# Optimization experiments

Measured on AMD Instinct MI355X. Metric: run time of the kernel, lower is better.

Reference implementation:

```python
import jax, jax.numpy as jnp
import numpy as np

B, S, HID = 2, 2048, 2048
NH, NKV, HD = 16, 4, 128  # num_heads, num_kv_heads, head_dim; kqv_size = NH*HD = 2048
KV_DIM = NKV * HD  # 512


def setup_inputs() -> dict:
    key = jax.random.key(0)
    ks = jax.random.split(key, 7)
    sc = 0.02
    return {
        "hidden_states": jax.random.normal(ks[0], (B, S, HID), dtype=jnp.float32),
        "Wq": jax.random.normal(ks[1], (NH * HD, HID), dtype=jnp.float32) * sc,
        "Wk": jax.random.normal(ks[2], (KV_DIM, HID), dtype=jnp.float32) * sc,
        "Wv": jax.random.normal(ks[3], (KV_DIM, HID), dtype=jnp.float32) * sc,
        "Wo": jax.random.normal(ks[4], (HID, NH * HD), dtype=jnp.float32) * sc,
        "bo": jnp.zeros((HID,), dtype=jnp.float32),
    }


def reference(hidden_states, Wq, Wk, Wv, Wo, bo):
    b, s, _ = hidden_states.shape
    # projections (nn.Linear: x @ W.T), no bias on q/k/v
    q = (hidden_states @ Wq.T).reshape(b, s, NH, HD).transpose(0, 2, 1, 3)   # [B,NH,S,HD]
    k = (hidden_states @ Wk.T).reshape(b, s, NKV, HD).transpose(0, 2, 1, 3)  # [B,NKV,S,HD]
    v = (hidden_states @ Wv.T).reshape(b, s, NKV, HD).transpose(0, 2, 1, 3)
    # GQA: query head h uses kv head h // (NH // NKV)
    g = NH // NKV
    k_rep = jnp.repeat(k, g, axis=1)  # [B,NH,S,HD]
    v_rep = jnp.repeat(v, g, axis=1)
    # float32 upcast, NO 1/sqrt(d) scaling (GPT-Neo style)
    qf = q.astype(jnp.float32)
    kf = k_rep.astype(jnp.float32)
    scores = jnp.einsum("bhqd,bhkd->bhqk", qf, kf)  # [B,NH,S,S]
    causal = jnp.tril(jnp.ones((s, s), dtype=bool))[None, None]
    neg = jnp.finfo(scores.dtype).min
    scores = jnp.where(causal, scores, neg)
    attn = jax.nn.softmax(scores, axis=-1).astype(v.dtype)  # dropout p=0 (eval)
    out = jnp.einsum("bhqk,bhkd->bhqd", attn, v_rep)         # [B,NH,S,HD]
    out = out.transpose(0, 2, 1, 3).reshape(b, s, NH * HD)
    return out @ Wo.T + bo
```

## Files before the change

### kernel.cpp

```cpp
#include <hip/hip_runtime.h>

typedef _Float16 f16;
typedef __attribute__((ext_vector_type(4))) _Float16 f16x4;
typedef __attribute__((ext_vector_type(8))) _Float16 f16x8;
typedef __attribute__((ext_vector_type(4))) float f32x4;

#define NB 2
#define NS 2048
#define NHID 2048
#define N_H 16
#define N_KV 4
#define N_HD 128

__device__ __forceinline__ void gload16(void* lds, const void* g) {
  __builtin_amdgcn_global_load_lds(
      (const __attribute__((address_space(1))) unsigned int*)g,
      (__attribute__((address_space(3))) unsigned int*)lds, 16, 0, 0);
}

__global__ __launch_bounds__(256) void cvt_kernel(const float* __restrict__ in,
                                                  f16* __restrict__ out, int n4) {
  int i = blockIdx.x * 256 + threadIdx.x;
  if (i >= n4) return;
  const float4 v = reinterpret_cast<const float4*>(in)[i];
  f16x4 o = {(f16)v.x, (f16)v.y, (f16)v.z, (f16)v.w};
  reinterpret_cast<f16x4*>(out)[i] = o;
}

__global__ __launch_bounds__(256) void cvt3_kernel(const float* __restrict__ a, int na4,
                                                   const float* __restrict__ b, int nb4,
                                                   const float* __restrict__ c, int nc4,
                                                   f16* __restrict__ out) {
  int i = blockIdx.x * 256 + threadIdx.x;
  if (i >= na4 + nb4 + nc4) return;
  const float* src;
  int j;
  if (i < na4) { src = a; j = i; }
  else if (i < na4 + nb4) { src = b; j = i - na4; }
  else { src = c; j = i - na4 - nb4; }
  const float4 v = reinterpret_cast<const float4*>(src)[j];
  f16x4 o = {(f16)v.x, (f16)v.y, (f16)v.z, (f16)v.w};
  reinterpret_cast<f16x4*>(out)[i] = o;
}

template <int MREP, int MODE>
__global__ __launch_bounds__(512, 2) void gemm8(
    const f16* __restrict__ A, const f16* __restrict__ Bm, const int K,
    f16* __restrict__ q_out, f16* __restrict__ k_out, f16* __restrict__ v_out,
    float* __restrict__ f_out, const float* __restrict__ bias) {
  constexpr int BM = MREP * 32;
  constexpr int GA = BM / 128;
  constexpr int G = GA + 2;
  constexpr int NPH = (MREP == 8) ? 2 : 1;
  constexpr int ATILE = BM * 32;
  constexpr int BTILE = 256 * 32;
  constexpr int BUF = ATILE + BTILE;
  __shared__ f16 lds[4 * BUF];

  const int t = threadIdx.x;
  const int l = t & 63, w = t >> 6;
  const int g = l >> 4, l15 = l & 15;
  const int wr = w >> 2, wc = w & 3;
  const int nb = blockIdx.x, mb = blockIdx.y;
  const int NT = K >> 5;

  const f16* Aorig = A + (size_t)(mb * BM) * K;
  const f16* Borig = Bm + (size_t)(nb * 256) * K;

  size_t offA[GA], offB[2];
#pragma unroll
  for (int gi = 0; gi < GA; ++gi) {
    int beta = gi * 8192 + t * 16;
    int r = ((beta >> 9) << 3) | ((beta >> 4) & 7);
    int c = (beta >> 7) & 3;
    offA[gi] = (size_t)r * K + c * 8;
  }
#pragma unroll
  for (int gj = 0; gj < 2; ++gj) {
    int beta = gj * 8192 + t * 16;
    int r = ((beta >> 9) << 3) | ((beta >> 4) & 7);
    int c = (beta >> 7) & 3;
    offB[gj] = (size_t)r * K + c * 8;
  }

  auto stage = [&](int kt, int gi) {
    f16* bufbase = lds + (kt & 3) * BUF;
    if (gi < GA) {
      gload16(bufbase + gi * 4096 + w * 512, Aorig + offA[gi] + kt * 32);
    } else {
      int gj = gi - GA;
      gload16(bufbase + ATILE + gj * 4096 + w * 512, Borig + offB[gj] + kt * 32);
    }
  };
  const int fragoff = ((l15 >> 3) << 8) + (g << 6) + ((l15 & 7) << 3);
  auto readA = [&](int kt, int mi) -> f16x8 {
    int R0 = wr * (MREP * 16) + mi * 16;
    return *reinterpret_cast<const f16x8*>(lds + (kt & 3) * BUF + R0 * 32 + fragoff);
  };
  auto readB = [&](int kt, int ni) -> f16x8 {
    int R0 = wc * 64 + ni * 16;
    return *reinterpret_cast<const f16x8*>(lds + (kt & 3) * BUF + ATILE + R0 * 32 + fragoff);
  };

  f32x4 acc[MREP][4] = {};

#pragma unroll
  for (int pt = 0; pt < 3; ++pt)
#pragma unroll
    for (int gi = 0; gi < G; ++gi) stage(pt, gi);
  if constexpr (MREP == 8) asm volatile("s_waitcnt vmcnt(8)" ::: "memory");
  else                     asm volatile("s_waitcnt vmcnt(6)" ::: "memory");
  __builtin_amdgcn_s_barrier();

  f16x8 bf[4];
  for (int kt = 0; kt < NT; ++kt) {
    const bool dostage = (kt + 3 < NT);
#pragma unroll
    for (int ph = 0; ph < NPH; ++ph) {
      f16x8 af[4];
#pragma unroll
      for (int mi = 0; mi < 4; ++mi) af[mi] = readA(kt, ph * 4 + mi);
      if (ph == 0) {
#pragma unroll
        for (int ni = 0; ni < 4; ++ni) bf[ni] = readB(kt, ni);
      }
      if (dostage) {
        if constexpr (NPH == 2) {
          stage(kt + 3, ph * 2);
          stage(kt + 3, ph * 2 + 1);
        } else {
          stage(kt + 3, 0);
          stage(kt + 3, 1);
          stage(kt + 3, 2);
        }
      }
      if (ph == NPH - 1) {
        if (kt + 3 < NT) {
          if constexpr (MREP == 8) asm volatile("s_waitcnt vmcnt(8)" ::: "memory");
          else                     asm volatile("s_waitcnt vmcnt(6)" ::: "memory");
        } else if (kt + 2 < NT) {
          if constexpr (MREP == 8) asm volatile("s_waitcnt vmcnt(4)" ::: "memory");
          else                     asm volatile("s_waitcnt vmcnt(3)" ::: "memory");
        } else if (kt + 1 < NT) {
          asm volatile("s_waitcnt vmcnt(0)" ::: "memory");
        }
      }
      __builtin_amdgcn_s_barrier();
      asm volatile("s_waitcnt lgkmcnt(0)" ::: "memory");
      __builtin_amdgcn_s_setprio(1);
#pragma unroll
      for (int mi = 0; mi < 4; ++mi)
#pragma unroll
        for (int ni = 0; ni < 4; ++ni)
          acc[ph * 4 + mi][ni] =
              __builtin_amdgcn_mfma_f32_16x16x32_f16(af[mi], bf[ni], acc[ph * 4 + mi][ni], 0, 0, 0);
      __builtin_amdgcn_s_setprio(0);
      __builtin_amdgcn_s_barrier();
    }
  }

#pragma unroll
  for (int mi = 0; mi < MREP; ++mi) {
    int m0 = mb * BM + wr * (MREP * 16) + mi * 16 + 4 * g;
#pragma unroll
    for (int ni = 0; ni < 4; ++ni) {
      int n = nb * 256 + wc * 64 + ni * 16 + l15;
#pragma unroll
      for (int r = 0; r < 4; ++r) {
        int mm = m0 + r;
        float val = acc[mi][ni][r];
        if (MODE == 0) {
          int b = mm >> 11, s = mm & (NS - 1);
          if (n < 2048) {
            int h = n >> 7, d = n & 127;
            q_out[(((size_t)(b * N_H + h)) * NS + s) * N_HD + d] = (f16)val;
          } else if (n < 2560) {
            int n2 = n - 2048, kvh = n2 >> 7, d = n2 & 127;
            k_out[(((size_t)(b * N_KV + kvh)) * NS + s) * N_HD + d] = (f16)val;
          } else {
            int n3 = n - 2560, kvh = n3 >> 7, d = n3 & 127;
            v_out[(((size_t)(b * N_KV + kvh)) * NS + s) * N_HD + d] = (f16)val;
          }
        } else {
          f_out[(size_t)mm * NHID + n] = val + bias[n];
        }
      }
    }
  }
}

__global__ __launch_bounds__(256) void transpose_v(const f16* __restrict__ V,
                                                   f16* __restrict__ Vt) {
  __shared__ f16 tt[64][72];
  int s0 = blockIdx.x * 64, d0 = blockIdx.y * 64, bk = blockIdx.z;
  const f16* Vp = V + (size_t)bk * NS * N_HD;
  f16* Vtp = Vt + (size_t)bk * N_HD * NS;
  int tid = threadIdx.x;
#pragma unroll
  for (int it = 0; it < 2; ++it) {
    int c = it * 256 + tid;
    int sr = c >> 3, dc = (c & 7) * 8;
    f16x8 v = *reinterpret_cast<const f16x8*>(Vp + (size_t)(s0 + sr) * N_HD + d0 + dc);
#pragma unroll
    for (int j = 0; j < 8; ++j) tt[dc + j][sr] = v[j];
  }
  __syncthreads();
#pragma unroll
  for (int it = 0; it < 2; ++it) {
    int c = it * 256 + tid;
    int dr = c >> 3, sc = (c & 7) * 8;
    f16x8 o;
#pragma unroll
    for (int j = 0; j < 8; ++j) o[j] = tt[dr][sc + j];
    *reinterpret_cast<f16x8*>(Vtp + (size_t)(d0 + dr) * NS + s0 + sc) = o;
  }
}

__device__ __forceinline__ void stage_kv(const f16* __restrict__ Kp,
                                         const f16* __restrict__ Vp,
                                         f16* Kl, f16* Vl, int kt, int w, int l) {
#pragma unroll
  for (int it = 0; it < 4; ++it) {
    int cb = (it * 4 + w) * 64;
    int c = cb + l;
    int krow = c >> 4, pch = c & 15;
    int sch = (pch & 8) | ((pch ^ krow) & 7);
    gload16(Kl + cb * 8, Kp + (size_t)(kt * 64 + krow) * N_HD + sch * 8);
  }
#pragma unroll
  for (int it = 0; it < 4; ++it) {
    int cb = (it * 4 + w) * 64;
    int c = cb + l;
    int drow = c >> 3, pch = c & 7;
    int sch = (pch ^ drow) & 7;
    gload16(Vl + cb * 8, Vp + (size_t)drow * NS + kt * 64 + sch * 8);
  }
}

__device__ __forceinline__ void attn_step(
    const f16x8* qf, f32x4* oacc, float* mrow, float* lrow, int q0, int kt,
    const f16* Kl, const f16* Vl, f16* Pw, int g, int l15, bool diag) {
  f32x4 sacc[4];
  __builtin_amdgcn_s_setprio(1);
#pragma unroll
  for (int nt = 0; nt < 4; ++nt) {
    f32x4 z = {0.f, 0.f, 0.f, 0.f};
#pragma unroll
    for (int ks = 0; ks < 4; ++ks) {
      int kr = nt * 16 + l15;
      int ch = ks * 4 + g;
      int sw = (ch & 8) | ((ch ^ kr) & 7);
      f16x8 kf = *reinterpret_cast<const f16x8*>(Kl + kr * 128 + sw * 8);
      z = __builtin_amdgcn_mfma_f32_16x16x32_f16(qf[ks], kf, z, 0, 0, 0);
    }
    sacc[nt] = z;
  }
  __builtin_amdgcn_s_setprio(0);

  float p[4][4], mx[4];
  bool need = false;
#pragma unroll
  for (int r = 0; r < 4; ++r) {
    int qg = q0 + r;
    float m = -3.0e38f;
#pragma unroll
    for (int nt = 0; nt < 4; ++nt) {
      float sv = sacc[nt][r];
      if (diag) {
        int kg = kt * 64 + nt * 16 + l15;
        if (kg > qg) sv = -3.0e38f;
      }
      p[nt][r] = sv;
      m = fmaxf(m, sv);
    }
#pragma unroll
    for (int off = 8; off >= 1; off >>= 1) m = fmaxf(m, __shfl_xor(m, off));
    mx[r] = m;
    need = need || (m > mrow[r] + 11.5f);
  }
  if (__any(need)) {
#pragma unroll
    for (int r = 0; r < 4; ++r) {
      float m2 = fmaxf(mrow[r], mx[r]);
      float alpha = __builtin_amdgcn_exp2f(mrow[r] - m2);
      mrow[r] = m2;
      lrow[r] *= alpha;
#pragma unroll
      for (int dt = 0; dt < 8; ++dt) oacc[dt][r] *= alpha;
    }
  }
#pragma unroll
  for (int r = 0; r < 4; ++r) {
    float rs = 0.f;
#pragma unroll
    for (int nt = 0; nt < 4; ++nt) {
      float pv = __builtin_amdgcn_exp2f(p[nt][r] - mrow[r]);
      p[nt][r] = pv;
      rs += pv;
    }
#pragma unroll
    for (int off = 8; off >= 1; off >>= 1) rs += __shfl_xor(rs, off);
    lrow[r] += rs;
  }

#pragma unroll
  for (int nt = 0; nt < 4; ++nt)
#pragma unroll
    for (int r = 0; r < 4; ++r) {
      int ql = 4 * g + r;
      int kp = nt * 16 + l15;
      int ch = kp >> 3;
      int idx = ql * 64 + (ch ^ (ql & 7)) * 8 + (kp & 7);
      Pw[idx] = (f16)p[nt][r];
    }
  asm volatile("s_waitcnt lgkmcnt(0)" ::: "memory");
  __builtin_amdgcn_sched_barrier(0);

  f16x8 pa[2];
#pragma unroll
  for (int ks2 = 0; ks2 < 2; ++ks2) {
    int ch = ks2 * 4 + g;
    pa[ks2] = *reinterpret_cast<const f16x8*>(&Pw[l15 * 64 + (ch ^ (l15 & 7)) * 8]);
  }
  __builtin_amdgcn_s_setprio(1);
#pragma unroll
  for (int dt = 0; dt < 8; ++dt)
#pragma unroll
    for (int ks2 = 0; ks2 < 2; ++ks2) {
      int d = dt * 16 + l15;
      int ch = ks2 * 4 + g;
      f16x8 vf = *reinterpret_cast<const f16x8*>(Vl + d * 64 + (ch ^ (d & 7)) * 8);
      oacc[dt] = __builtin_amdgcn_mfma_f32_16x16x32_f16(pa[ks2], vf, oacc[dt], 0, 0, 0);
    }
  __builtin_amdgcn_s_setprio(0);
}

__global__ __launch_bounds__(256, 2) void attn_kernel(
    const f16* __restrict__ Q, const f16* __restrict__ K,
    const f16* __restrict__ Vt, f16* __restrict__ O) {
  __shared__ f16 Klds[2][64 * 128];
  __shared__ f16 Vlds[2][128 * 64];
  __shared__ f16 Plds[4][16 * 64];
  const int t = threadIdx.x, l = t & 63, w = t >> 6;
  const int g = l >> 4, l15 = l & 15;
  const int pi = blockIdx.x;
  const int qtA = pi, qtB = 31 - pi;
  const int bh = blockIdx.y;
  const int b = bh >> 4, h = bh & 15;
  const int kvh = h >> 2;
  const f16* Qp = Q + ((size_t)(b * N_H + h)) * NS * N_HD;
  const f16* Kp = K + ((size_t)(b * N_KV + kvh)) * NS * N_HD;
  const f16* Vp = Vt + ((size_t)(b * N_KV + kvh)) * N_HD * NS;

  const f16 l2e = (f16)1.44269504f;
  f16x8 qfA[4], qfB[4];
  const int qrA = qtA * 64 + w * 16 + l15;
  const int qrB = qtB * 64 + w * 16 + l15;
#pragma unroll
  for (int ks = 0; ks < 4; ++ks) {
    qfA[ks] = *reinterpret_cast<const f16x8*>(Qp + (size_t)qrA * N_HD + ks * 32 + g * 8);
    qfB[ks] = *reinterpret_cast<const f16x8*>(Qp + (size_t)qrB * N_HD + ks * 32 + g * 8);
#pragma unroll
    for (int j = 0; j < 8; ++j) { qfA[ks][j] *= l2e; qfB[ks][j] *= l2e; }
  }

  f32x4 oA[8] = {}, oB[8] = {};
  float mA[4], lAr[4], mB[4], lBr[4];
#pragma unroll
  for (int r = 0; r < 4; ++r) {
    mA[r] = -3.0e38f; lAr[r] = 0.f;
    mB[r] = -3.0e38f; lBr[r] = 0.f;
  }
  const int q0A = qtA * 64 + w * 16 + 4 * g;
  const int q0B = qtB * 64 + w * 16 + 4 * g;

  const int nkt = qtB + 1;
  stage_kv(Kp, Vp, Klds[0], Vlds[0], 0, w, l);
  asm volatile("s_waitcnt vmcnt(0)" ::: "memory");
  __syncthreads();
  int cur = 0;
  for (int kt = 0; kt < nkt; ++kt) {
    if (kt + 1 < nkt)
      stage_kv(Kp, Vp, Klds[cur ^ 1], Vlds[cur ^ 1], kt + 1, w, l);
    attn_step(qfB, oB, mB, lBr, q0B, kt, Klds[cur], Vlds[cur], Plds[w], g, l15, kt == qtB);
    if (kt <= qtA)
      attn_step(qfA, oA, mA, lAr, q0A, kt, Klds[cur], Vlds[cur], Plds[w], g, l15, kt == qtA);
    asm volatile("s_waitcnt vmcnt(0)" ::: "memory");
    __syncthreads();
    cur ^= 1;
  }

#pragma unroll
  for (int r = 0; r < 4; ++r) {
    float invB = 1.0f / lBr[r];
    f16* orowB = O + (size_t)(b * NS + q0B + r) * NHID + h * N_HD;
#pragma unroll
    for (int dt = 0; dt < 8; ++dt) orowB[dt * 16 + l15] = (f16)(oB[dt][r] * invB);
    float invA = 1.0f / lAr[r];
    f16* orowA = O + (size_t)(b * NS + q0A + r) * NHID + h * N_HD;
#pragma unroll
    for (int dt = 0; dt < 8; ++dt) orowA[dt * 16 + l15] = (f16)(oA[dt][r] * invA);
  }
}

extern "C" void kernel_launch(void* const* d_in, const int* in_sizes, int n_in,
                              void* d_out, int out_size, void* d_ws, size_t ws_size,
                              hipStream_t stream) {
  const float* hs = (const float*)d_in[0];
  const float* Wq = (const float*)d_in[1];
  const float* Wk = (const float*)d_in[2];
  const float* Wv = (const float*)d_in[3];
  const float* Wo = (const float*)d_in[4];
  const float* bo = (const float*)d_in[5];
  float* out = (float*)d_out;

  char* ws = (char*)d_ws;
  f16* Xh   = (f16*)(ws);
  f16* Wqkv = (f16*)(ws + 16777216);
  f16* Woh  = (f16*)(ws + 29360128);
  f16* Qb   = (f16*)(ws + 37748736);
  f16* Kb   = (f16*)(ws + 54525952);
  f16* Vb   = (f16*)(ws + 58720256);
  f16* Vtb  = (f16*)(ws + 62914560);
  f16* Ob   = Xh;

  cvt_kernel<<<8192, 256, 0, stream>>>(hs, Xh, 2097152);
  cvt3_kernel<<<6144, 256, 0, stream>>>(Wq, 1048576, Wk, 262144, Wv, 262144, Wqkv);
  cvt_kernel<<<4096, 256, 0, stream>>>(Wo, Woh, 1048576);

  gemm8<8, 0><<<dim3(12, 16), 512, 0, stream>>>(Xh, Wqkv, 2048, Qb, Kb, Vb, nullptr, nullptr);
  transpose_v<<<dim3(32, 2, 8), 256, 0, stream>>>(Vb, Vtb);
  attn_kernel<<<dim3(16, 32), 256, 0, stream>>>(Qb, Kb, Vtb, Ob);
  gemm8<4, 1><<<dim3(8, 32), 512, 0, stream>>>(Ob, Woh, 2048, nullptr, nullptr, nullptr, out, bo);
}
```

Measured before the change: 239.8 us.

## Fuse conversions, add 256-block QKV GEMM, swizzle grids, simplify attention softmax

Merges the three fp32-to-fp16 conversion launches into one kernel. Replaces the QKV projection with a dedicated GEMM using 256x192 tiles and double-buffered 64-wide K steps, so the launch is 256 blocks. Remaps block indices in the QKV GEMM, output GEMM and attention kernel so that blocks sharing operand tiles or a KV head are launched together, aiming for better L2 reuse. In attention, the lazy-rescale branch is dropped in favour of always rescaling, row sums are computed with an MFMA against a ones vector instead of shuffles, and the setprio hints are removed. The trade-off is extra rescale work on every tile and a shallower load pipeline in the new GEMM.

```diff
diff --git a/kernel.cpp b/kernel.cpp
--- a/kernel.cpp
+++ b/kernel.cpp
@@ -18,35 +18,123 @@
       (__attribute__((address_space(3))) unsigned int*)lds, 16, 0, 0);
 }
 
-__global__ __launch_bounds__(256) void cvt_kernel(const float* __restrict__ in,
-                                                  f16* __restrict__ out, int n4) {
+__global__ __launch_bounds__(256) void cvt_all(
+    const float* __restrict__ hs, const float* __restrict__ Wq,
+    const float* __restrict__ Wk, const float* __restrict__ Wv,
+    const float* __restrict__ Wo, f16* __restrict__ Xh,
+    f16* __restrict__ Wqkv, f16* __restrict__ Woh) {
   int i = blockIdx.x * 256 + threadIdx.x;
-  if (i >= n4) return;
-  const float4 v = reinterpret_cast<const float4*>(in)[i];
-  f16x4 o = {(f16)v.x, (f16)v.y, (f16)v.z, (f16)v.w};
-  reinterpret_cast<f16x4*>(out)[i] = o;
-}
-
-__global__ __launch_bounds__(256) void cvt3_kernel(const float* __restrict__ a, int na4,
-                                                   const float* __restrict__ b, int nb4,
-                                                   const float* __restrict__ c, int nc4,
-                                                   f16* __restrict__ out) {
-  int i = blockIdx.x * 256 + threadIdx.x;
-  if (i >= na4 + nb4 + nc4) return;
   const float* src;
+  f16* dst;
   int j;
-  if (i < na4) { src = a; j = i; }
-  else if (i < na4 + nb4) { src = b; j = i - na4; }
-  else { src = c; j = i - na4 - nb4; }
+  if (i < 2097152)      { src = hs; dst = Xh;             j = i; }
+  else if (i < 3145728) { src = Wq; dst = Wqkv;           j = i - 2097152; }
+  else if (i < 3407872) { src = Wk; dst = Wqkv + 4194304; j = i - 3145728; }
+  else if (i < 3670016) { src = Wv; dst = Wqkv + 5242880; j = i - 3407872; }
+  else                  { src = Wo; dst = Woh;            j = i - 3670016; }
   const float4 v = reinterpret_cast<const float4*>(src)[j];
   f16x4 o = {(f16)v.x, (f16)v.y, (f16)v.z, (f16)v.w};
-  reinterpret_cast<f16x4*>(out)[i] = o;
+  reinterpret_cast<f16x4*>(dst)[j] = o;
+}
+
+__global__ __launch_bounds__(512, 2) void gemm_qkv(
+    const f16* __restrict__ A, const f16* __restrict__ Bm,
+    f16* __restrict__ q_out, f16* __restrict__ k_out, f16* __restrict__ v_out) {
+  constexpr int K = 2048;
+  __shared__ f16 lds[2][28672];
+  const int t = threadIdx.x;
+  const int l = t & 63, w = t >> 6;
+  const int g = l >> 4, l15 = l & 15;
+  const int wr = w >> 2, wc = w & 3;
+  const int orig = blockIdx.x;
+  const int x = orig & 7, loc = orig >> 3;
+  const int mb = (x & 3) * 4 + (loc & 3);
+  const int nb = (x >> 2) * 8 + (loc >> 2);
+  const f16* Ab = A + (size_t)(mb * 256) * K;
+  const f16* Bb = Bm + (size_t)(nb * 192) * K;
+
+  const int rA = ((t >> 5) << 3) | (t & 7);
+  const int cA = (t >> 3) & 3;
+  const int t2 = t & 255;
+  const int rB2 = ((t2 >> 5) << 3) | (t2 & 7);
+  const int cB2 = (t2 >> 3) & 3;
+
+  auto stage = [&](int kt) {
+    f16* buf = lds[kt & 1];
+#pragma unroll
+    for (int h = 0; h < 2; ++h) {
+#pragma unroll
+      for (int gi = 0; gi < 2; ++gi)
+        gload16(buf + h * 8192 + gi * 4096 + w * 512,
+                Ab + (size_t)(gi * 128 + rA) * K + kt * 64 + h * 32 + cA * 8);
+      gload16(buf + 16384 + h * 6144 + w * 512,
+              Bb + (size_t)rA * K + kt * 64 + h * 32 + cA * 8);
+      if (t < 256)
+        gload16(buf + 16384 + h * 6144 + 4096 + w * 512,
+                Bb + (size_t)(128 + rB2) * K + kt * 64 + h * 32 + cB2 * 8);
+    }
+  };
+  const int fragoff = ((l15 >> 3) << 8) + (g << 6) + ((l15 & 7) << 3);
+
+  f32x4 acc[8][3] = {};
+
+  stage(0);
+  asm volatile("s_waitcnt vmcnt(0)" ::: "memory");
+  __builtin_amdgcn_s_barrier();
+
+  for (int kt = 0; kt < 32; ++kt) {
+    if (kt + 1 < 32) stage(kt + 1);
+    const f16* buf = lds[kt & 1];
+#pragma unroll
+    for (int h = 0; h < 2; ++h) {
+      f16x8 af[8], bf[3];
+#pragma unroll
+      for (int mi = 0; mi < 8; ++mi)
+        af[mi] = *reinterpret_cast<const f16x8*>(buf + h * 8192 + (wr * 128 + mi * 16) * 32 + fragoff);
+#pragma unroll
+      for (int ni = 0; ni < 3; ++ni)
+        bf[ni] = *reinterpret_cast<const f16x8*>(buf + 16384 + h * 6144 + (wc * 48 + ni * 16) * 32 + fragoff);
+      __builtin_amdgcn_s_setprio(1);
+#pragma unroll
+      for (int mi = 0; mi < 8; ++mi)
+#pragma unroll
+        for (int ni = 0; ni < 3; ++ni)
+          acc[mi][ni] = __builtin_amdgcn_mfma_f32_16x16x32_f16(af[mi], bf[ni], acc[mi][ni], 0, 0, 0);
+      __builtin_amdgcn_s_setprio(0);
+    }
+    if (kt + 1 < 32) asm volatile("s_waitcnt vmcnt(0)" ::: "memory");
+    __builtin_amdgcn_s_barrier();
+  }
+
+#pragma unroll
+  for (int mi = 0; mi < 8; ++mi) {
+    int m0 = mb * 256 + wr * 128 + mi * 16 + 4 * g;
+#pragma unroll
+    for (int ni = 0; ni < 3; ++ni) {
+      int n = nb * 192 + wc * 48 + ni * 16 + l15;
+#pragma unroll
+      for (int r = 0; r < 4; ++r) {
+        int mm = m0 + r;
+        float val = acc[mi][ni][r];
+        int b = mm >> 11, s = mm & (NS - 1);
+        if (n < 2048) {
+          int h = n >> 7, d = n & 127;
+          q_out[(((size_t)(b * N_H + h)) * NS + s) * N_HD + d] = (f16)val;
+        } else if (n < 2560) {
+          int n2 = n - 2048, kvh = n2 >> 7, d = n2 & 127;
+          k_out[(((size_t)(b * N_KV + kvh)) * NS + s) * N_HD + d] = (f16)val;
+        } else {
+          int n3 = n - 2560, kvh = n3 >> 7, d = n3 & 127;
+          v_out[(((size_t)(b * N_KV + kvh)) * NS + s) * N_HD + d] = (f16)val;
+        }
+      }
+    }
+  }
 }
 
 template <int MREP, int MODE>
 __global__ __launch_bounds__(512, 2) void gemm8(
     const f16* __restrict__ A, const f16* __restrict__ Bm, const int K,
-    f16* __restrict__ q_out, f16* __restrict__ k_out, f16* __restrict__ v_out,
     float* __restrict__ f_out, const float* __restrict__ bias) {
   constexpr int BM = MREP * 32;
   constexpr int GA = BM / 128;
@@ -61,7 +149,10 @@
   const int l = t & 63, w = t >> 6;
   const int g = l >> 4, l15 = l & 15;
   const int wr = w >> 2, wc = w & 3;
-  const int nb = blockIdx.x, mb = blockIdx.y;
+  const int orig = blockIdx.x;
+  const int x = orig & 7, loc = orig >> 3;
+  int mb, nb;
+  mb = (x & 3) * 8 + (loc & 7); nb = (x >> 2) * 4 + (loc >> 3);
   const int NT = K >> 5;
 
   const f16* Aorig = A + (size_t)(mb * BM) * K;
@@ -108,8 +199,7 @@
   for (int pt = 0; pt < 3; ++pt)
 #pragma unroll
     for (int gi = 0; gi < G; ++gi) stage(pt, gi);
-  if constexpr (MREP == 8) asm volatile("s_waitcnt vmcnt(8)" ::: "memory");
-  else                     asm volatile("s_waitcnt vmcnt(6)" ::: "memory");
+  asm volatile("s_waitcnt vmcnt(6)" ::: "memory");
   __builtin_amdgcn_s_barrier();
 
   f16x8 bf[4];
@@ -125,25 +215,14 @@
         for (int ni = 0; ni < 4; ++ni) bf[ni] = readB(kt, ni);
       }
       if (dostage) {
-        if constexpr (NPH == 2) {
-          stage(kt + 3, ph * 2);
-          stage(kt + 3, ph * 2 + 1);
-        } else {
-          stage(kt + 3, 0);
-          stage(kt + 3, 1);
-          stage(kt + 3, 2);
-        }
+        stage(kt + 3, 0);
+        stage(kt + 3, 1);
+        stage(kt + 3, 2);
       }
       if (ph == NPH - 1) {
-        if (kt + 3 < NT) {
-          if constexpr (MREP == 8) asm volatile("s_waitcnt vmcnt(8)" ::: "memory");
-          else                     asm volatile("s_waitcnt vmcnt(6)" ::: "memory");
-        } else if (kt + 2 < NT) {
-          if constexpr (MREP == 8) asm volatile("s_waitcnt vmcnt(4)" ::: "memory");
-          else                     asm volatile("s_waitcnt vmcnt(3)" ::: "memory");
-        } else if (kt + 1 < NT) {
-          asm volatile("s_waitcnt vmcnt(0)" ::: "memory");
-        }
+        if (kt + 3 < NT)      asm volatile("s_waitcnt vmcnt(6)" ::: "memory");
+        else if (kt + 2 < NT) asm volatile("s_waitcnt vmcnt(3)" ::: "memory");
+        else if (kt + 1 < NT) asm volatile("s_waitcnt vmcnt(0)" ::: "memory");
       }
       __builtin_amdgcn_s_barrier();
       asm volatile("s_waitcnt lgkmcnt(0)" ::: "memory");
@@ -167,23 +246,7 @@
       int n = nb * 256 + wc * 64 + ni * 16 + l15;
 #pragma unroll
       for (int r = 0; r < 4; ++r) {
-        int mm = m0 + r;
-        float val = acc[mi][ni][r];
-        if (MODE == 0) {
-          int b = mm >> 11, s = mm & (NS - 1);
-          if (n < 2048) {
-            int h = n >> 7, d = n & 127;
-            q_out[(((size_t)(b * N_H + h)) * NS + s) * N_HD + d] = (f16)val;
-          } else if (n < 2560) {
-            int n2 = n - 2048, kvh = n2 >> 7, d = n2 & 127;
-            k_out[(((size_t)(b * N_KV + kvh)) * NS + s) * N_HD + d] = (f16)val;
-          } else {
-            int n3 = n - 2560, kvh = n3 >> 7, d = n3 & 127;
-            v_out[(((size_t)(b * N_KV + kvh)) * NS + s) * N_HD + d] = (f16)val;
-          }
-        } else {
-          f_out[(size_t)mm * NHID + n] = val + bias[n];
-        }
+        f_out[(size_t)(m0 + r) * NHID + n] = acc[mi][ni][r] + bias[n];
       }
     }
   }
@@ -241,7 +304,6 @@
     const f16x8* qf, f32x4* oacc, float* mrow, float* lrow, int q0, int kt,
     const f16* Kl, const f16* Vl, f16* Pw, int g, int l15, bool diag) {
   f32x4 sacc[4];
-  __builtin_amdgcn_s_setprio(1);
 #pragma unroll
   for (int nt = 0; nt < 4; ++nt) {
     f32x4 z = {0.f, 0.f, 0.f, 0.f};
@@ -255,10 +317,8 @@
     }
     sacc[nt] = z;
   }
-  __builtin_amdgcn_s_setprio(0);
-
-  float p[4][4], mx[4];
-  bool need = false;
+
+  float p[4][4];
 #pragma unroll
   for (int r = 0; r < 4; ++r) {
     int qg = q0 + r;
@@ -275,32 +335,15 @@
     }
 #pragma unroll
     for (int off = 8; off >= 1; off >>= 1) m = fmaxf(m, __shfl_xor(m, off));
-    mx[r] = m;
-    need = need || (m > mrow[r] + 11.5f);
-  }
-  if (__any(need)) {
-#pragma unroll
-    for (int r = 0; r < 4; ++r) {
-      float m2 = fmaxf(mrow[r], mx[r]);
-      float alpha = __builtin_amdgcn_exp2f(mrow[r] - m2);
-      mrow[r] = m2;
-      lrow[r] *= alpha;
-#pragma unroll
-      for (int dt = 0; dt < 8; ++dt) oacc[dt][r] *= alpha;
-    }
-  }
-#pragma unroll
-  for (int r = 0; r < 4; ++r) {
-    float rs = 0.f;
-#pragma unroll
-    for (int nt = 0; nt < 4; ++nt) {
-      float pv = __builtin_amdgcn_exp2f(p[nt][r] - mrow[r]);
-      p[nt][r] = pv;
-      rs += pv;
-    }
-#pragma unroll
-    for (int off = 8; off >= 1; off >>= 1) rs += __shfl_xor(rs, off);
-    lrow[r] += rs;
+    float m2 = fmaxf(mrow[r], m);
+    float alpha = __builtin_amdgcn_exp2f(mrow[r] - m2);
+    mrow[r] = m2;
+    lrow[r] *= alpha;
+#pragma unroll
+    for (int nt = 0; nt < 4; ++nt)
+      p[nt][r] = __builtin_amdgcn_exp2f(p[nt][r] - m2);
+#pragma unroll
+    for (int dt = 0; dt < 8; ++dt) oacc[dt][r] *= alpha;
   }
 
 #pragma unroll
@@ -322,7 +365,12 @@
     int ch = ks2 * 4 + g;
     pa[ks2] = *reinterpret_cast<const f16x8*>(&Pw[l15 * 64 + (ch ^ (l15 & 7)) * 8]);
   }
-  __builtin_amdgcn_s_setprio(1);
+  const f16x8 ones = {(f16)1.f, (f16)1.f, (f16)1.f, (f16)1.f,
+                      (f16)1.f, (f16)1.f, (f16)1.f, (f16)1.f};
+  f32x4 lacc = {0.f, 0.f, 0.f, 0.f};
+#pragma unroll
+  for (int ks2 = 0; ks2 < 2; ++ks2)
+    lacc = __builtin_amdgcn_mfma_f32_16x16x32_f16(pa[ks2], ones, lacc, 0, 0, 0);
 #pragma unroll
   for (int dt = 0; dt < 8; ++dt)
 #pragma unroll
@@ -332,7 +380,8 @@
       f16x8 vf = *reinterpret_cast<const f16x8*>(Vl + d * 64 + (ch ^ (d & 7)) * 8);
       oacc[dt] = __builtin_amdgcn_mfma_f32_16x16x32_f16(pa[ks2], vf, oacc[dt], 0, 0, 0);
     }
-  __builtin_amdgcn_s_setprio(0);
+#pragma unroll
+  for (int r = 0; r < 4; ++r) lrow[r] += lacc[r];
 }
 
 __global__ __launch_bounds__(256, 2) void attn_kernel(
@@ -343,11 +392,12 @@
   __shared__ f16 Plds[4][16 * 64];
   const int t = threadIdx.x, l = t & 63, w = t >> 6;
   const int g = l >> 4, l15 = l & 15;
-  const int pi = blockIdx.x;
+  const int orig = blockIdx.x;
+  const int x = orig & 7, loc = orig >> 3;
+  const int b = x >> 2, kvh = x & 3;
+  const int h = kvh * 4 + (loc & 3);
+  const int pi = loc >> 2;
   const int qtA = pi, qtB = 31 - pi;
-  const int bh = blockIdx.y;
-  const int b = bh >> 4, h = bh & 15;
-  const int kvh = h >> 2;
   const f16* Qp = Q + ((size_t)(b * N_H + h)) * NS * N_HD;
   const f16* Kp = K + ((size_t)(b * N_KV + kvh)) * NS * N_HD;
   const f16* Vp = Vt + ((size_t)(b * N_KV + kvh)) * N_HD * NS;
@@ -424,12 +474,9 @@
   f16* Vtb  = (f16*)(ws + 62914560);
   f16* Ob   = Xh;
 
-  cvt_kernel<<<8192, 256, 0, stream>>>(hs, Xh, 2097152);
-  cvt3_kernel<<<6144, 256, 0, stream>>>(Wq, 1048576, Wk, 262144, Wv, 262144, Wqkv);
-  cvt_kernel<<<4096, 256, 0, stream>>>(Wo, Woh, 1048576);
-
-  gemm8<8, 0><<<dim3(12, 16), 512, 0, stream>>>(Xh, Wqkv, 2048, Qb, Kb, Vb, nullptr, nullptr);
+  cvt_all<<<18432, 256, 0, stream>>>(hs, Wq, Wk, Wv, Wo, Xh, Wqkv, Woh);
+  gemm_qkv<<<256, 512, 0, stream>>>(Xh, Wqkv, Qb, Kb, Vb);
   transpose_v<<<dim3(32, 2, 8), 256, 0, stream>>>(Vb, Vtb);
-  attn_kernel<<<dim3(16, 32), 256, 0, stream>>>(Qb, Kb, Vtb, Ob);
-  gemm8<4, 1><<<dim3(8, 32), 512, 0, stream>>>(Ob, Woh, 2048, nullptr, nullptr, nullptr, out, bo);
-}
+  attn_kernel<<<512, 256, 0, stream>>>(Qb, Kb, Vtb, Ob);
+  gemm8<4, 1><<<256, 512, 0, stream>>>(Ob, Woh, 2048, out, bo);
+}
```

Result: faster. 216.1 us (-9.9%).
